# Performance work log

Measured on AMD Instinct MI355X. Metric: run time of the kernel, lower is better.

## Reference

```python
import jax, jax.numpy as jnp
import numpy as np


def _chord_mask(n):
    # Chord-protocol sparsity: mask[i, i] = 1 and mask[i, (i + 2**j) % n] = 1
    m = np.zeros((n, n), dtype=np.float32)
    idx = np.arange(n)
    m[idx, idx] = 1.0
    for j in range(int(np.log2(n))):
        m[idx, (idx + 2 ** j) % n] = 1.0
    return jnp.asarray(m)


def setup_inputs() -> dict:
    key = jax.random.key(0)
    ks = jax.random.split(key, 8)
    B, n_vec, n_dim = 16, 1024, 64
    n_hidden, n_W, n_class = 32, 10, 10
    data = jax.random.normal(ks[0], (B, n_vec, n_dim), dtype=jnp.float32)
    s1 = 1.0 / np.sqrt(n_dim)
    s2 = 1.0 / np.sqrt(n_hidden)
    s3 = 1.0 / np.sqrt(n_vec * n_dim)
    fW1 = jax.random.uniform(ks[1], (n_W, n_dim, n_hidden), jnp.float32, -s1, s1)
    fb1 = jax.random.uniform(ks[2], (n_W, n_hidden), jnp.float32, -s1, s1)
    fW2 = jax.random.uniform(ks[3], (n_W, n_hidden, n_vec), jnp.float32, -s2, s2)
    fb2 = jax.random.uniform(ks[4], (n_W, n_vec), jnp.float32, -s2, s2)
    final_W = jax.random.uniform(ks[5], (n_vec * n_dim, n_class), jnp.float32, -s3, s3)
    final_b = jax.random.uniform(ks[6], (n_class,), jnp.float32, -s3, s3)
    return {"data": data, "fW1": fW1, "fb1": fb1, "fW2": fW2, "fb2": fb2,
            "final_W": final_W, "final_b": final_b}


def reference(data, fW1, fb1, fW2, fb2, final_W, final_b):
    B, n_vec, n_dim = data.shape
    n_W = fW1.shape[0]
    mask = _chord_mask(n_vec)  # [n_vec, n_vec], static constant
    V = data
    residual = V
    # fs[::-1] -> iterate layers in reverse order
    for i in range(n_W - 1, -1, -1):
        h = jax.nn.gelu(jnp.einsum('bnd,dh->bnh', data, fW1[i]) + fb1[i],
                        approximate=False)
        W = jnp.einsum('bnh,hm->bnm', h, fW2[i]) + fb2[i]  # [B, n_vec, n_vec]
        W = W * mask
        V = jnp.einsum('bnm,bmd->bnd', W, V) + residual
        residual = V  # residual_every=True
    flat = V.reshape(B, n_vec * n_dim)
    return flat @ final_W + final_b
```

## Files before the change

### kernel.cpp

```cpp
#include <hip/hip_runtime.h>

#define BATCH 16
#define NVEC 1024
#define NDIM 64
#define NHID 32
#define NW   10
#define NCLS 10
#define NOFF 11
#define WPAD 12
#define NCHUNK (NDIM / 4)
#define W2PAD 36

__global__ __launch_bounds__(256) void k_weights(
    const float* __restrict__ data,
    const float* __restrict__ fW1,
    const float* __restrict__ fb1,
    const float* __restrict__ fW2,
    const float* __restrict__ fb2,
    float* __restrict__ Wsp)
{
    const int i = blockIdx.y;
    const int nbase = blockIdx.x * 8;
    const int t = threadIdx.x;
    const int b  = t & 15;
    const int jq = (t >> 4) & 3;
    const int nl = t >> 6;
    const int j0 = jq * 8;

    __shared__ __align__(16) float sW1[NDIM * NHID];
    __shared__ float sb1[NHID];
    __shared__ __align__(16) float sW2r[64 * W2PAD];
    __shared__ float sb2[64];
    __shared__ __align__(16) float rws[128 * WPAD];

    {
        const float4* w1v = (const float4*)(fW1 + (size_t)i * NDIM * NHID);
        float4* s4 = (float4*)sW1;
        #pragma unroll
        for (int k = t; k < NDIM * NHID / 4; k += 256) s4[k] = w1v[k];
        if (t < NHID) sb1[t] = fb1[i * NHID + t];

        const int j  = t >> 3;
        const int s0 = t & 7;
        const float* w2 = fW2 + ((size_t)i * NHID + j) * NVEC;
        #pragma unroll
        for (int c = 0; c < 8; ++c) {
            int s = s0 + c * 8;
            int k = (s < 24) ? s : ((32 << ((s - 24) >> 3)) + ((s - 24) & 7));
            int m = (nbase + k) & (NVEC - 1);
            sW2r[s * W2PAD + j] = w2[m];
        }
        if (t < 64) {
            int s = t;
            int k = (s < 24) ? s : ((32 << ((s - 24) >> 3)) + ((s - 24) & 7));
            int m = (nbase + k) & (NVEC - 1);
            sb2[s] = fb2[(size_t)i * NVEC + m];
        }
        for (int k = t; k < 128; k += 256) rws[k * WPAD + (WPAD - 1)] = 0.0f;
    }
    __syncthreads();

    float h[2][8];
    #pragma unroll
    for (int r = 0; r < 2; ++r)
        #pragma unroll
        for (int jj = 0; jj < 8; ++jj) h[r][jj] = sb1[j0 + jj];

    const int n0 = nbase + nl * 2;
    const float4* arow0 = (const float4*)(data + ((size_t)(b * NVEC) + n0) * NDIM);
    const float4* arow1 = (const float4*)(data + ((size_t)(b * NVEC) + n0 + 1) * NDIM);

    #pragma unroll 4
    for (int g = 0; g < 16; ++g) {
        float4 a0 = arow0[g];
        float4 a1 = arow1[g];
        float as0[4] = {a0.x, a0.y, a0.z, a0.w};
        float as1[4] = {a1.x, a1.y, a1.z, a1.w};
        #pragma unroll
        for (int dk = 0; dk < 4; ++dk) {
            const float4* wp = (const float4*)(&sW1[(g * 4 + dk) * NHID + j0]);
            float4 w0 = wp[0], w1 = wp[1];
            const float wf[8] = {w0.x, w0.y, w0.z, w0.w, w1.x, w1.y, w1.z, w1.w};
            #pragma unroll
            for (int jj = 0; jj < 8; ++jj) {
                h[0][jj] += as0[dk] * wf[jj];
                h[1][jj] += as1[dk] * wf[jj];
            }
        }
    }

    #pragma unroll
    for (int r = 0; r < 2; ++r)
        #pragma unroll
        for (int jj = 0; jj < 8; ++jj) {
            float x = h[r][jj];
            h[r][jj] = 0.5f * x * (1.0f + erff(x * 0.70710678118654752f));
        }

    const int rbase = nl * 2;
    #pragma unroll
    for (int r = 0; r < 2; ++r) {
        #pragma unroll
        for (int o = 0; o < NOFF; ++o) {
            int slot;
            if (o == 0) slot = rbase + r;
            else {
                int off = 1 << (o - 1);
                slot = (off <= 16) ? (rbase + r + off)
                                   : (24 + 8 * (o - 6) + rbase + r);
            }
            const float4* gp = (const float4*)(sW2r + slot * W2PAD + j0);
            float4 g0 = gp[0], g1 = gp[1];
            float w = h[r][0] * g0.x + h[r][1] * g0.y + h[r][2] * g0.z + h[r][3] * g0.w
                    + h[r][4] * g1.x + h[r][5] * g1.y + h[r][6] * g1.z + h[r][7] * g1.w;
            w += __shfl_xor(w, 16, 64);
            w += __shfl_xor(w, 32, 64);
            if (jq == (o & 3))
                rws[(b * 8 + rbase + r) * WPAD + o] = w + sb2[slot];
        }
    }
    __syncthreads();

    {
        const float4* rv = (const float4*)rws;
        #pragma unroll
        for (int k = t; k < 128 * 3; k += 256) {
            int row = k / 3, comp = k - row * 3;
            int bb = row >> 3, nloc = row & 7;
            float4* dst = (float4*)(Wsp +
                ((size_t)(i * BATCH + bb) * NVEC + nbase + nloc) * WPAD + comp * 4);
            *dst = rv[k];
        }
    }
}

__global__ __launch_bounds__(1024) void k_chain(
    const float* __restrict__ data,
    const float* __restrict__ Wsp,
    const float* __restrict__ Wf,
    float* __restrict__ part)
{
    const int lin   = blockIdx.x;
    const int xcd   = lin & 7;
    const int slot  = lin >> 3;
    const int b     = (xcd << 1) | (slot >> 4);
    const int chunk = slot & 15;
    const int d0    = chunk * 4;
    const int n     = threadIdx.x;

    __shared__ float4 bufA[NVEC];
    __shared__ float4 bufB[NVEC];

    float4 vown = *(const float4*)(data + ((size_t)(b * NVEC) + n) * NDIM + d0);
    bufA[n] = vown;

    const float4* wp = (const float4*)(Wsp + ((size_t)((NW - 1) * BATCH + b) * NVEC + n) * WPAD);
    float4 wa = wp[0], wb4 = wp[1], wc = wp[2];
    __syncthreads();

    float4* cur = bufA;
    float4* nxt = bufB;

    for (int l = 0; l < NW; ++l) {
        float4 na, nb, nc;
        if (l < NW - 1) {
            const float4* wpn = (const float4*)(
                Wsp + ((size_t)((NW - 2 - l) * BATCH + b) * NVEC + n) * WPAD);
            na = wpn[0]; nb = wpn[1]; nc = wpn[2];
        }
        const float wgt[12] = {wa.x, wa.y, wa.z, wa.w,
                               wb4.x, wb4.y, wb4.z, wb4.w,
                               wc.x, wc.y, wc.z, wc.w};
        float4 v0 = vown;
        float4 acc;
        acc.x = v0.x + wgt[0] * v0.x;
        acc.y = v0.y + wgt[0] * v0.y;
        acc.z = v0.z + wgt[0] * v0.z;
        acc.w = v0.w + wgt[0] * v0.w;
        #pragma unroll
        for (int o = 1; o < NOFF; ++o) {
            int off = 1 << (o - 1);
            float4 vv = cur[(n + off) & (NVEC - 1)];
            acc.x += wgt[o] * vv.x; acc.y += wgt[o] * vv.y;
            acc.z += wgt[o] * vv.z; acc.w += wgt[o] * vv.w;
        }
        nxt[n] = acc;
        vown = acc;
        __syncthreads();
        float4* tmp = cur; cur = nxt; nxt = tmp;
        if (l < NW - 1) { wa = na; wb4 = nb; wc = nc; }
    }

    float p[NCLS];
    #pragma unroll
    for (int c = 0; c < NCLS; ++c) p[c] = 0.0f;
    {
        float vs[4] = {vown.x, vown.y, vown.z, vown.w};
        const float4* wfv = (const float4*)(Wf + ((size_t)(n * NDIM + d0)) * NCLS);
        float wf[40];
        #pragma unroll
        for (int k = 0; k < 10; ++k) {
            float4 u = wfv[k];
            wf[k * 4 + 0] = u.x; wf[k * 4 + 1] = u.y;
            wf[k * 4 + 2] = u.z; wf[k * 4 + 3] = u.w;
        }
        #pragma unroll
        for (int d = 0; d < 4; ++d)
            #pragma unroll
            for (int cls = 0; cls < NCLS; ++cls)
                p[cls] += vs[d] * wf[d * NCLS + cls];
    }

    const int lane = n & 63, wv = n >> 6;
    float* sred = (float*)nxt;
    #pragma unroll
    for (int cls = 0; cls < NCLS; ++cls) {
        float v = p[cls];
        #pragma unroll
        for (int s = 32; s > 0; s >>= 1) v += __shfl_down(v, s, 64);
        if (lane == 0) sred[wv * NCLS + cls] = v;
    }
    __syncthreads();
    if (n < NCLS) {
        float s = 0.0f;
        #pragma unroll
        for (int w = 0; w < 16; ++w) s += sred[w * NCLS + n];
        part[(size_t)(b * NCHUNK + chunk) * NCLS + n] = s;
    }
}

__global__ __launch_bounds__(256) void k_finish(
    const float* __restrict__ part, const float* __restrict__ bias,
    float* __restrict__ out)
{
    int t = threadIdx.x;
    if (t < BATCH * NCLS) {
        int b = t / NCLS, cls = t % NCLS;
        float s = bias[cls];
        #pragma unroll
        for (int ch = 0; ch < NCHUNK; ++ch)
            s += part[(size_t)(b * NCHUNK + ch) * NCLS + cls];
        out[t] = s;
    }
}

extern "C" void kernel_launch(void* const* d_in, const int* in_sizes, int n_in,
                              void* d_out, int out_size, void* d_ws, size_t ws_size,
                              hipStream_t stream) {
    const float* data = (const float*)d_in[0];
    const float* fW1  = (const float*)d_in[1];
    const float* fb1  = (const float*)d_in[2];
    const float* fW2  = (const float*)d_in[3];
    const float* fb2  = (const float*)d_in[4];
    const float* fWf  = (const float*)d_in[5];
    const float* fbf  = (const float*)d_in[6];
    float* out = (float*)d_out;

    float* ws   = (float*)d_ws;
    float* Wsp  = ws;
    float* part = Wsp + (size_t)NW * BATCH * NVEC * WPAD;

    k_weights<<<dim3(NVEC / 8, NW), 256, 0, stream>>>(
        data, fW1, fb1, fW2, fb2, Wsp);
    k_chain<<<dim3(NCHUNK * BATCH), 1024, 0, stream>>>(data, Wsp, fWf, part);
    k_finish<<<dim3(1), 256, 0, stream>>>(part, fbf, out);
}
```

Before: 120.7 us.

## Process 16 rows per weights block with 4 rows per thread and lane-local j split

The weights kernel now handles 16 rows per block instead of 8, with each thread computing 4 rows rather than 2. This halves the block count and amortizes the per-block fW1 and fW2 shared-memory staging over more rows. The thread mapping puts the hidden-quarter index in the low lane bits, so the cross-quarter reduction uses shuffles at distance 1 and 2 instead of 16 and 32. The cost is higher register pressure (32 hidden accumulators per thread) and more shared memory per block, mitigated by a launch-bounds occupancy hint.

```diff
diff --git a/kernel.cpp b/kernel.cpp
--- a/kernel.cpp
+++ b/kernel.cpp
@@ -10,8 +10,10 @@
 #define WPAD 12
 #define NCHUNK (NDIM / 4)
 #define W2PAD 36
-
-__global__ __launch_bounds__(256) void k_weights(
+#define NROW 16
+#define NSLOT 112
+
+__global__ __launch_bounds__(256, 4) void k_weights(
     const float* __restrict__ data,
     const float* __restrict__ fW1,
     const float* __restrict__ fb1,
@@ -20,18 +22,18 @@
     float* __restrict__ Wsp)
 {
     const int i = blockIdx.y;
-    const int nbase = blockIdx.x * 8;
+    const int nbase = blockIdx.x * NROW;
     const int t = threadIdx.x;
-    const int b  = t & 15;
-    const int jq = (t >> 4) & 3;
+    const int jq = t & 3;
+    const int b  = (t >> 2) & 15;
     const int nl = t >> 6;
     const int j0 = jq * 8;
 
     __shared__ __align__(16) float sW1[NDIM * NHID];
     __shared__ float sb1[NHID];
-    __shared__ __align__(16) float sW2r[64 * W2PAD];
-    __shared__ float sb2[64];
-    __shared__ __align__(16) float rws[128 * WPAD];
+    __shared__ __align__(16) float sW2r[NSLOT * W2PAD];
+    __shared__ float sb2[NSLOT];
+    __shared__ __align__(16) float rws[NROW * BATCH * WPAD];
 
     {
         const float4* w1v = (const float4*)(fW1 + (size_t)i * NDIM * NHID);
@@ -44,38 +46,41 @@
         const int s0 = t & 7;
         const float* w2 = fW2 + ((size_t)i * NHID + j) * NVEC;
         #pragma unroll
-        for (int c = 0; c < 8; ++c) {
+        for (int c = 0; c < NSLOT / 8; ++c) {
             int s = s0 + c * 8;
-            int k = (s < 24) ? s : ((32 << ((s - 24) >> 3)) + ((s - 24) & 7));
+            int k = (s < 32) ? s : ((32 << ((s - 32) >> 4)) + ((s - 32) & 15));
             int m = (nbase + k) & (NVEC - 1);
             sW2r[s * W2PAD + j] = w2[m];
         }
-        if (t < 64) {
+        if (t < NSLOT) {
             int s = t;
-            int k = (s < 24) ? s : ((32 << ((s - 24) >> 3)) + ((s - 24) & 7));
+            int k = (s < 32) ? s : ((32 << ((s - 32) >> 4)) + ((s - 32) & 15));
             int m = (nbase + k) & (NVEC - 1);
             sb2[s] = fb2[(size_t)i * NVEC + m];
         }
-        for (int k = t; k < 128; k += 256) rws[k * WPAD + (WPAD - 1)] = 0.0f;
-    }
-    __syncthreads();
-
-    float h[2][8];
-    #pragma unroll
-    for (int r = 0; r < 2; ++r)
+        for (int k = t; k < NROW * BATCH; k += 256) rws[k * WPAD + (WPAD - 1)] = 0.0f;
+    }
+    __syncthreads();
+
+    float h[4][8];
+    #pragma unroll
+    for (int r = 0; r < 4; ++r)
         #pragma unroll
         for (int jj = 0; jj < 8; ++jj) h[r][jj] = sb1[j0 + jj];
 
-    const int n0 = nbase + nl * 2;
-    const float4* arow0 = (const float4*)(data + ((size_t)(b * NVEC) + n0) * NDIM);
-    const float4* arow1 = (const float4*)(data + ((size_t)(b * NVEC) + n0 + 1) * NDIM);
-
-    #pragma unroll 4
+    const int n0 = nbase + nl * 4;
+    const float4* rowp = (const float4*)(data + ((size_t)(b * NVEC) + n0) * NDIM);
+
+    #pragma unroll 2
     for (int g = 0; g < 16; ++g) {
-        float4 a0 = arow0[g];
-        float4 a1 = arow1[g];
-        float as0[4] = {a0.x, a0.y, a0.z, a0.w};
-        float as1[4] = {a1.x, a1.y, a1.z, a1.w};
+        float4 a0 = rowp[g];
+        float4 a1 = rowp[16 + g];
+        float4 a2 = rowp[32 + g];
+        float4 a3 = rowp[48 + g];
+        const float as[4][4] = {{a0.x, a0.y, a0.z, a0.w},
+                                {a1.x, a1.y, a1.z, a1.w},
+                                {a2.x, a2.y, a2.z, a2.w},
+                                {a3.x, a3.y, a3.z, a3.w}};
         #pragma unroll
         for (int dk = 0; dk < 4; ++dk) {
             const float4* wp = (const float4*)(&sW1[(g * 4 + dk) * NHID + j0]);
@@ -83,23 +88,25 @@
             const float wf[8] = {w0.x, w0.y, w0.z, w0.w, w1.x, w1.y, w1.z, w1.w};
             #pragma unroll
             for (int jj = 0; jj < 8; ++jj) {
-                h[0][jj] += as0[dk] * wf[jj];
-                h[1][jj] += as1[dk] * wf[jj];
+                h[0][jj] += as[0][dk] * wf[jj];
+                h[1][jj] += as[1][dk] * wf[jj];
+                h[2][jj] += as[2][dk] * wf[jj];
+                h[3][jj] += as[3][dk] * wf[jj];
             }
         }
     }
 
     #pragma unroll
-    for (int r = 0; r < 2; ++r)
+    for (int r = 0; r < 4; ++r)
         #pragma unroll
         for (int jj = 0; jj < 8; ++jj) {
             float x = h[r][jj];
             h[r][jj] = 0.5f * x * (1.0f + erff(x * 0.70710678118654752f));
         }
 
-    const int rbase = nl * 2;
-    #pragma unroll
-    for (int r = 0; r < 2; ++r) {
+    const int rbase = nl * 4;
+    #pragma unroll
+    for (int r = 0; r < 4; ++r) {
         #pragma unroll
         for (int o = 0; o < NOFF; ++o) {
             int slot;
@@ -107,16 +114,16 @@
             else {
                 int off = 1 << (o - 1);
                 slot = (off <= 16) ? (rbase + r + off)
-                                   : (24 + 8 * (o - 6) + rbase + r);
+                                   : (32 + 16 * (o - 6) + rbase + r);
             }
             const float4* gp = (const float4*)(sW2r + slot * W2PAD + j0);
             float4 g0 = gp[0], g1 = gp[1];
             float w = h[r][0] * g0.x + h[r][1] * g0.y + h[r][2] * g0.z + h[r][3] * g0.w
                     + h[r][4] * g1.x + h[r][5] * g1.y + h[r][6] * g1.z + h[r][7] * g1.w;
-            w += __shfl_xor(w, 16, 64);
-            w += __shfl_xor(w, 32, 64);
+            w += __shfl_xor(w, 1, 64);
+            w += __shfl_xor(w, 2, 64);
             if (jq == (o & 3))
-                rws[(b * 8 + rbase + r) * WPAD + o] = w + sb2[slot];
+                rws[(b * NROW + rbase + r) * WPAD + o] = w + sb2[slot];
         }
     }
     __syncthreads();
@@ -124,11 +131,11 @@
     {
         const float4* rv = (const float4*)rws;
         #pragma unroll
-        for (int k = t; k < 128 * 3; k += 256) {
+        for (int k = t; k < NROW * BATCH * 3; k += 256) {
             int row = k / 3, comp = k - row * 3;
-            int bb = row >> 3, nloc = row & 7;
+            int bb = row >> 4, rr = row & 15;
             float4* dst = (float4*)(Wsp +
-                ((size_t)(i * BATCH + bb) * NVEC + nbase + nloc) * WPAD + comp * 4);
+                ((size_t)(i * BATCH + bb) * NVEC + nbase + rr) * WPAD + comp * 4);
             *dst = rv[k];
         }
     }
@@ -260,7 +267,7 @@
     float* Wsp  = ws;
     float* part = Wsp + (size_t)NW * BATCH * NVEC * WPAD;
 
-    k_weights<<<dim3(NVEC / 8, NW), 256, 0, stream>>>(
+    k_weights<<<dim3(NVEC / NROW, NW), 256, 0, stream>>>(
         data, fW1, fb1, fW2, fb2, Wsp);
     k_chain<<<dim3(NCHUNK * BATCH), 1024, 0, stream>>>(data, Wsp, fWf, part);
     k_finish<<<dim3(1), 256, 0, stream>>>(part, fbf, out);
```

Measured after the change: 115.8 us. 4.1% less time.
